# Kernel optimization log

Measured on AMD Instinct MI355X. Metric: run time of the kernel, lower is better.

The kernel has to match this reference:

```python
import jax, jax.numpy as jnp
import numpy as np

K = 500        # conv kernel == stride (non-overlapping windows)
C_IN = 8       # embedding dim
C_OUT = 128    # conv out channels
VOCAB = 257    # 256 byte values + padding idx 256


def setup_inputs() -> dict:
    key = jax.random.key(0)
    ks = jax.random.split(key, 10)
    B, L = 8, 1 << 20
    x = jax.random.randint(ks[0], (B, L), 0, VOCAB, dtype=jnp.int32)
    emb = 0.1 * jax.random.normal(ks[1], (VOCAB, C_IN), jnp.float32)
    emb = emb.at[VOCAB - 1].set(0.0)  # padding_idx=256 -> zero row
    lim_c = 1.0 / np.sqrt(C_IN * K)
    w1 = jax.random.uniform(ks[2], (C_OUT, C_IN, K), jnp.float32, -lim_c, lim_c)
    b1 = jax.random.uniform(ks[3], (C_OUT,), jnp.float32, -lim_c, lim_c)
    w2 = jax.random.uniform(ks[4], (C_OUT, C_IN, K), jnp.float32, -lim_c, lim_c)
    b2 = jax.random.uniform(ks[5], (C_OUT,), jnp.float32, -lim_c, lim_c)
    lim_d = 1.0 / np.sqrt(C_OUT)
    wd1 = jax.random.uniform(ks[6], (C_OUT, C_OUT), jnp.float32, -lim_d, lim_d)
    bd1 = jax.random.uniform(ks[7], (C_OUT,), jnp.float32, -lim_d, lim_d)
    wd2 = jax.random.uniform(ks[8], (1, C_OUT), jnp.float32, -lim_d, lim_d)
    bd2 = jax.random.uniform(ks[9], (1,), jnp.float32, -lim_d, lim_d)
    return {"x": x, "emb": emb, "w1": w1, "b1": b1, "w2": w2, "b2": b2,
            "wd1": wd1, "bd1": bd1, "wd2": wd2, "bd2": bd2}


def reference(x, emb, w1, b1, w2, b2, wd1, bd1, wd2, bd2):
    B, L = x.shape
    T = (L - K) // K + 1  # valid conv output length (== L // K here)
    xe = emb[x]                                  # [B, L, 8]  embedding lookup
    win = xe[:, : T * K].reshape(B, T, K, C_IN)  # [B, T, 500, 8] non-overlap windows
    c1 = jnp.einsum('btke,oek->bto', win, w1) + b1  # [B, T, 128]
    c2 = jnp.einsum('btke,oek->bto', win, w2) + b2
    gated = jax.nn.relu(c1) * jax.nn.sigmoid(c2)    # gated activation
    pooled = jnp.max(gated, axis=1)                 # global max pool over time -> [B, 128]
    h = jax.nn.relu(pooled @ wd1.T + bd1)           # [B, 128]
    out = jax.nn.sigmoid(h @ wd2.T + bd2)           # [B, 1]
    return out
```

## Files before the change

kernel.cpp:

```cpp
#include <hip/hip_runtime.h>

#define BATCH   8
#define LSEQ    1048576
#define KCONV   500
#define TWIN    2097
#define MROWS   16776
#define KDIM    4000
#define NDIM    256
#define COUT    128
#define VOCAB   257
#define VOCABP  256

#define BMR     80
#define NTILE   210
#define SLABP   20
#define NSLAB   25
#define NG      125
#define PLANE   (NDIM * 32)
#define AROWSH  168
#define STAGEN  (BMR * SLABP)

#define WTF_OFF   0ull
#define WTF_BYTES ((size_t)NG * PLANE * 2)
#define POOL_OFF  (WTF_OFF + WTF_BYTES)

typedef __attribute__((ext_vector_type(8))) __bf16 bf16x8;
typedef __attribute__((ext_vector_type(4))) float  floatx4;

__device__ inline unsigned short f2bf(float f) {
    union { float f; unsigned u; } c; c.f = f;
    return (unsigned short)((c.u + 0x7FFFu + ((c.u >> 16) & 1u)) >> 16);
}
__device__ inline unsigned pack2(float lo, float hi) {
    return (unsigned)f2bf(lo) | ((unsigned)f2bf(hi) << 16);
}

#define LDS_BARRIER() asm volatile("s_waitcnt lgkmcnt(0)\n\ts_barrier" ::: "memory")

__global__ __launch_bounds__(256) void wprep_kernel(const float* __restrict__ w1,
                                                    const float* __restrict__ w2,
                                                    unsigned short* __restrict__ Wtf,
                                                    float* __restrict__ pool) {
    const int n   = blockIdx.x;
    const int tid = threadIdx.x;
    __shared__ float tile[KDIM];
    const float* src = (n < COUT) ? (w1 + (size_t)n * KDIM)
                                  : (w2 + (size_t)(n - COUT) * KDIM);
    for (int i = tid; i < KDIM; i += 256) tile[i] = src[i];
    __syncthreads();
    for (int i = tid; i < KDIM; i += 256) {
        int g = i >> 5, kk = i & 31;
        Wtf[(size_t)g * PLANE + n * 32 + kk] = f2bf(tile[(i & 7) * KCONV + (i >> 3)]);
    }
    if (n == 0 && tid < BATCH * COUT / 2)
        ((float2*)pool)[tid] = float2{0.f, 0.f};
}

__global__ __launch_bounds__(512) void gemm_kernel(const int* __restrict__ x,
                                                   const float* __restrict__ emb,
                                                   const unsigned short* __restrict__ Wtf,
                                                   const float* __restrict__ b1,
                                                   const float* __restrict__ b2,
                                                   float* __restrict__ pool) {
    __shared__ unsigned short tableL[VOCAB * 8];
    __shared__ unsigned short As[2][BMR * AROWSH];

    const int tid  = threadIdx.x;
    const int lane = tid & 63;
    const int wv   = tid >> 6;
    const int m0   = blockIdx.x * BMR;
    const int r16  = lane & 15;
    const int q    = lane >> 4;

    if (tid < VOCAB) {
        const float4* er = (const float4*)(emb + tid * 8);
        float4 a = er[0], b = er[1];
        uint4 u;
        u.x = pack2(a.x, a.y); u.y = pack2(a.z, a.w);
        u.z = pack2(b.x, b.y); u.w = pack2(b.z, b.w);
        *(uint4*)(tableL + tid * 8) = u;
    }

    const int* xptr[4];
    int        loff[4];
    bool       sval[4];
#pragma unroll
    for (int l = 0; l < 4; ++l) {
        int idx = tid + 512 * l;
        sval[l] = (idx < STAGEN);
        int ic  = sval[l] ? idx : 0;
        int row = ic / SLABP;
        int pos = ic - row * SLABP;
        int am  = m0 + row;
        bool av = sval[l] && (am < MROWS);
        sval[l] = av;
        int amc = av ? am : 0;
        int b   = amc / TWIN;
        int t   = amc - b * TWIN;
        xptr[l] = x + ((size_t)b * LSEQ + (size_t)t * KCONV + pos);
        loff[l] = row * AROWSH + pos * 8;
    }

    const int o = wv * 16 + r16;
    const size_t boff0 = (size_t)o * 32 + q * 8;
    const size_t boff1 = (size_t)(o + 128) * 32 + q * 8;

    floatx4 acc[5][2];
#pragma unroll
    for (int i = 0; i < 5; ++i) { acc[i][0] = floatx4{0,0,0,0}; acc[i][1] = floatx4{0,0,0,0}; }

    int xv[4];
#pragma unroll
    for (int l = 0; l < 4; ++l) xv[l] = sval[l] ? xptr[l][0] : VOCABP;
    __syncthreads();

#pragma unroll
    for (int l = 0; l < 4; ++l) {
        if (l == 3 && tid >= STAGEN - 3 * 512) break;
        uint4 g = *(const uint4*)(tableL + xv[l] * 8);
        *(uint4*)((unsigned short*)As + loff[l]) = g;
    }
#pragma unroll
    for (int l = 0; l < 4; ++l) if (sval[l]) xv[l] = xptr[l][SLABP];
    LDS_BARRIER();

    bf16x8 bc0[2], bc1[2], bc2[2] = {};
    bc0[0] = *(const bf16x8*)(Wtf + boff0);
    bc0[1] = *(const bf16x8*)(Wtf + boff1);
    bc1[0] = *(const bf16x8*)(Wtf + PLANE + boff0);
    bc1[1] = *(const bf16x8*)(Wtf + PLANE + boff1);

    int buf = 0;
    for (int s = 0; s < NSLAB; ++s) {
        if (s + 1 < NSLAB) {
            unsigned short* d = (unsigned short*)As + (buf ^ 1) * (BMR * AROWSH);
#pragma unroll
            for (int l = 0; l < 4; ++l) {
                if (l == 3 && tid >= STAGEN - 3 * 512) break;
                uint4 g = *(const uint4*)(tableL + xv[l] * 8);
                *(uint4*)(d + loff[l]) = g;
            }
        }
        if (s + 2 < NSLAB) {
#pragma unroll
            for (int l = 0; l < 4; ++l)
                if (sval[l]) xv[l] = xptr[l][(s + 2) * SLABP];
        }

        const unsigned short* Asb = (const unsigned short*)As + buf * (BMR * AROWSH);
#pragma unroll
        for (int kt = 0; kt < 5; ++kt) {
            const int g = s * 5 + kt;
            if (g + 2 < NG) {
                const unsigned short* Wp = Wtf + (size_t)(g + 2) * PLANE;
                bc2[0] = *(const bf16x8*)(Wp + boff0);
                bc2[1] = *(const bf16x8*)(Wp + boff1);
            }
            bf16x8 af[5];
#pragma unroll
            for (int i = 0; i < 5; ++i)
                af[i] = *(const bf16x8*)(Asb + (i * 16 + r16) * AROWSH + (kt * 4 + q) * 8);
#pragma unroll
            for (int i = 0; i < 5; ++i) {
                acc[i][0] = __builtin_amdgcn_mfma_f32_16x16x32_bf16(af[i], bc0[0], acc[i][0], 0, 0, 0);
                acc[i][1] = __builtin_amdgcn_mfma_f32_16x16x32_bf16(af[i], bc0[1], acc[i][1], 0, 0, 0);
            }
            bc0[0] = bc1[0]; bc0[1] = bc1[1];
            bc1[0] = bc2[0]; bc1[1] = bc2[1];
        }
        LDS_BARRIER();
        buf ^= 1;
    }

    const float b1v = b1[o], b2v = b2[o];
    float cur = 0.0f;
    int curb  = (m0 + q * 4) / TWIN;
#pragma unroll
    for (int i = 0; i < 5; ++i) {
#pragma unroll
        for (int rg = 0; rg < 4; ++rg) {
            const int row = m0 + i * 16 + q * 4 + rg;
            if (row < MROWS) {
                const int bb = row / TWIN;
                if (bb != curb) {
                    atomicMax((int*)&pool[curb * COUT + o], __float_as_int(cur));
                    cur = 0.0f; curb = bb;
                }
                const float c1 = acc[i][0][rg] + b1v;
                const float c2 = acc[i][1][rg] + b2v;
                const float g  = fmaxf(c1, 0.0f) / (1.0f + __expf(-c2));
                cur = fmaxf(cur, g);
            }
        }
    }
    atomicMax((int*)&pool[curb * COUT + o], __float_as_int(cur));
}

__global__ __launch_bounds__(128) void head_kernel(const float* __restrict__ pool,
                                                   const float* __restrict__ wd1,
                                                   const float* __restrict__ bd1,
                                                   const float* __restrict__ wd2,
                                                   const float* __restrict__ bd2,
                                                   float* __restrict__ out) {
    __shared__ float red[BATCH][COUT];
    int j = threadIdx.x;
    float wj = wd2[j];
#pragma unroll
    for (int b = 0; b < BATCH; ++b) {
        float s = bd1[j];
        for (int i = 0; i < COUT; ++i) s += pool[b * COUT + i] * wd1[j * COUT + i];
        red[b][j] = fmaxf(s, 0.0f) * wj;
    }
    __syncthreads();
    if (j < BATCH) {
        float s = 0.0f;
        for (int i = 0; i < COUT; ++i) s += red[j][i];
        out[j] = 1.0f / (1.0f + expf(-(s + bd2[0])));
    }
}

extern "C" void kernel_launch(void* const* d_in, const int* in_sizes, int n_in,
                              void* d_out, int out_size, void* d_ws, size_t ws_size,
                              hipStream_t stream) {
    const int*   x   = (const int*)d_in[0];
    const float* emb = (const float*)d_in[1];
    const float* w1  = (const float*)d_in[2];
    const float* b1  = (const float*)d_in[3];
    const float* w2  = (const float*)d_in[4];
    const float* b2  = (const float*)d_in[5];
    const float* wd1 = (const float*)d_in[6];
    const float* bd1 = (const float*)d_in[7];
    const float* wd2 = (const float*)d_in[8];
    const float* bd2 = (const float*)d_in[9];
    float* out = (float*)d_out;

    unsigned short* Wtf  = (unsigned short*)((char*)d_ws + WTF_OFF);
    float*          pool = (float*)((char*)d_ws + POOL_OFF);

    wprep_kernel<<<dim3(NDIM), dim3(256), 0, stream>>>(w1, w2, Wtf, pool);
    gemm_kernel<<<dim3(NTILE), dim3(512), 0, stream>>>(x, emb, Wtf, b1, b2, pool);
    head_kernel<<<dim3(1), dim3(128), 0, stream>>>(pool, wd1, bd1, wd2, bd2, out);
}
```

Baseline: 176.1 us.

## Fuse head MLP into GEMM via last-block ticket and prefetch A fragments

Removes the separate head kernel launch. The GEMM kernel now takes a ticket from an atomic counter stored after the pool buffer, and the last block to finish reads the pooled maxima and computes the dense head itself. It also double-buffers the LDS A-fragment loads so the next k-step is read while the current MFMAs run, and adds a min-blocks hint of 2 to launch bounds. The cost is extra register pressure, and the head work runs on only one block at the tail.

```diff
diff --git a/kernel.cpp b/kernel.cpp
--- a/kernel.cpp
+++ b/kernel.cpp
@@ -1,4 +1,5 @@
 #include <hip/hip_runtime.h>
+#include <limits.h>
 
 #define BATCH   8
 #define LSEQ    1048576
@@ -52,16 +53,21 @@
         int g = i >> 5, kk = i & 31;
         Wtf[(size_t)g * PLANE + n * 32 + kk] = f2bf(tile[(i & 7) * KCONV + (i >> 3)]);
     }
-    if (n == 0 && tid < BATCH * COUT / 2)
-        ((float2*)pool)[tid] = float2{0.f, 0.f};
-}
-
-__global__ __launch_bounds__(512) void gemm_kernel(const int* __restrict__ x,
-                                                   const float* __restrict__ emb,
-                                                   const unsigned short* __restrict__ Wtf,
-                                                   const float* __restrict__ b1,
-                                                   const float* __restrict__ b2,
-                                                   float* __restrict__ pool) {
+    if (n == 0)
+        for (int i = tid; i < BATCH * COUT + 1; i += 256) pool[i] = 0.0f;
+}
+
+__global__ __launch_bounds__(512, 2) void gemm_kernel(const int* __restrict__ x,
+                                                      const float* __restrict__ emb,
+                                                      const unsigned short* __restrict__ Wtf,
+                                                      const float* __restrict__ b1,
+                                                      const float* __restrict__ b2,
+                                                      float* __restrict__ pool,
+                                                      const float* __restrict__ wd1,
+                                                      const float* __restrict__ bd1,
+                                                      const float* __restrict__ wd2,
+                                                      const float* __restrict__ bd2,
+                                                      float* __restrict__ out) {
     __shared__ unsigned short tableL[VOCAB * 8];
     __shared__ unsigned short As[2][BMR * AROWSH];
 
@@ -148,22 +154,28 @@
         }
 
         const unsigned short* Asb = (const unsigned short*)As + buf * (BMR * AROWSH);
+        bf16x8 afp[2][5];
+#pragma unroll
+        for (int i = 0; i < 5; ++i)
+            afp[0][i] = *(const bf16x8*)(Asb + (i * 16 + r16) * AROWSH + q * 8);
 #pragma unroll
         for (int kt = 0; kt < 5; ++kt) {
+            if (kt < 4) {
+#pragma unroll
+                for (int i = 0; i < 5; ++i)
+                    afp[(kt + 1) & 1][i] =
+                        *(const bf16x8*)(Asb + (i * 16 + r16) * AROWSH + ((kt + 1) * 4 + q) * 8);
+            }
             const int g = s * 5 + kt;
             if (g + 2 < NG) {
                 const unsigned short* Wp = Wtf + (size_t)(g + 2) * PLANE;
                 bc2[0] = *(const bf16x8*)(Wp + boff0);
                 bc2[1] = *(const bf16x8*)(Wp + boff1);
             }
-            bf16x8 af[5];
-#pragma unroll
-            for (int i = 0; i < 5; ++i)
-                af[i] = *(const bf16x8*)(Asb + (i * 16 + r16) * AROWSH + (kt * 4 + q) * 8);
 #pragma unroll
             for (int i = 0; i < 5; ++i) {
-                acc[i][0] = __builtin_amdgcn_mfma_f32_16x16x32_bf16(af[i], bc0[0], acc[i][0], 0, 0, 0);
-                acc[i][1] = __builtin_amdgcn_mfma_f32_16x16x32_bf16(af[i], bc0[1], acc[i][1], 0, 0, 0);
+                acc[i][0] = __builtin_amdgcn_mfma_f32_16x16x32_bf16(afp[kt & 1][i], bc0[0], acc[i][0], 0, 0, 0);
+                acc[i][1] = __builtin_amdgcn_mfma_f32_16x16x32_bf16(afp[kt & 1][i], bc0[1], acc[i][1], 0, 0, 0);
             }
             bc0[0] = bc1[0]; bc0[1] = bc1[1];
             bc1[0] = bc2[0]; bc1[1] = bc2[1];
@@ -194,28 +206,33 @@
         }
     }
     atomicMax((int*)&pool[curb * COUT + o], __float_as_int(cur));
-}
-
-__global__ __launch_bounds__(128) void head_kernel(const float* __restrict__ pool,
-                                                   const float* __restrict__ wd1,
-                                                   const float* __restrict__ bd1,
-                                                   const float* __restrict__ wd2,
-                                                   const float* __restrict__ bd2,
-                                                   float* __restrict__ out) {
-    __shared__ float red[BATCH][COUT];
-    int j = threadIdx.x;
-    float wj = wd2[j];
-#pragma unroll
-    for (int b = 0; b < BATCH; ++b) {
-        float s = bd1[j];
-        for (int i = 0; i < COUT; ++i) s += pool[b * COUT + i] * wd1[j * COUT + i];
-        red[b][j] = fmaxf(s, 0.0f) * wj;
-    }
-    __syncthreads();
-    if (j < BATCH) {
-        float s = 0.0f;
-        for (int i = 0; i < COUT; ++i) s += red[j][i];
-        out[j] = 1.0f / (1.0f + expf(-(s + bd2[0])));
+
+    __shared__ unsigned int tick;
+    __threadfence();
+    __syncthreads();
+    if (tid == 0) tick = atomicAdd((unsigned int*)&pool[BATCH * COUT], 1u);
+    __syncthreads();
+    if (tick == NTILE - 1) {
+        float* scratch = (float*)&As[0][0];
+        float* pl   = scratch;
+        float* hred = scratch + BATCH * COUT;
+        for (int i = tid; i < BATCH * COUT; i += 512) {
+            int old = atomicMax((int*)&pool[i], INT_MIN);
+            pl[i] = __int_as_float(old);
+        }
+        __syncthreads();
+        for (int p = tid; p < BATCH * COUT; p += 512) {
+            const int b = p >> 7, j = p & 127;
+            float s = bd1[j];
+            for (int i = 0; i < COUT; ++i) s += pl[b * COUT + i] * wd1[j * COUT + i];
+            hred[p] = fmaxf(s, 0.0f) * wd2[j];
+        }
+        __syncthreads();
+        if (tid < BATCH) {
+            float s = 0.0f;
+            for (int i = 0; i < COUT; ++i) s += hred[tid * COUT + i];
+            out[tid] = 1.0f / (1.0f + expf(-(s + bd2[0])));
+        }
     }
 }
 
@@ -238,6 +255,6 @@
     float*          pool = (float*)((char*)d_ws + POOL_OFF);
 
     wprep_kernel<<<dim3(NDIM), dim3(256), 0, stream>>>(w1, w2, Wtf, pool);
-    gemm_kernel<<<dim3(NTILE), dim3(512), 0, stream>>>(x, emb, Wtf, b1, b2, pool);
-    head_kernel<<<dim3(1), dim3(128), 0, stream>>>(pool, wd1, bd1, wd2, bd2, out);
-}
+    gemm_kernel<<<dim3(NTILE), dim3(512), 0, stream>>>(x, emb, Wtf, b1, b2, pool,
+                                                       wd1, bd1, wd2, bd2, out);
+}
```

Result: slower. 187.1 us (+6.2%).
